# Optimization experiments

Hardware: AMD Instinct MI355X
Metric: run time of the kernel (lower is better)

## Reference

```python
import jax, jax.numpy as jnp
import numpy as np

EPS = jnp.float16(1e-8)

def setup_inputs() -> dict:
    key = jax.random.key(0)
    k1, k2, k3, k4 = jax.random.split(key, 4)
    B, S, D_IN, D_OUT = 4, 2048, 4096, 4096
    x = jax.random.normal(k1, (B, S, D_IN), dtype=jnp.float16)
    weight = jax.random.randint(k2, (D_OUT, D_IN), -127, 127, dtype=jnp.int32).astype(jnp.int8)
    weight_scales = (jax.random.uniform(k3, (D_OUT,), dtype=jnp.float32) * 0.02 + 0.001).astype(jnp.float16)
    bias = (jax.random.normal(k4, (1, D_OUT), dtype=jnp.float32) * 0.01).astype(jnp.float16)
    return {"x": x, "weight": weight, "weight_scales": weight_scales, "bias": bias}

def fake_quant_per_token(x):
    # per-token absmax fake quant to int8 range, stays fp16
    scales = jnp.max(jnp.abs(x), axis=-1, keepdims=True) / jnp.float16(127.0)
    scales = jnp.maximum(scales, EPS)
    return jnp.round(x / scales) * scales

def reference(x, weight, weight_scales, bias):
    # dequantize int8 weight with per-output-channel scales -> fp16 [out, in]
    w_fp16 = weight.astype(jnp.float16) * weight_scales[:, None]
    xq = fake_quant_per_token(x)
    # y = xq @ w^T + bias  : [B, S, out]
    y = jnp.einsum('bsi,oi->bso', xq, w_fp16) + bias
    return y
```

## Files before the change

kernel.cpp:

```cpp
#include <hip/hip_runtime.h>
#include <hip/hip_fp16.h>
#include <stdint.h>

#define M_TOK 8192
#define KD 4096
#define ND 4096

using i32x4  = __attribute__((ext_vector_type(4))) int;
using i32x16 = __attribute__((ext_vector_type(16))) int;

typedef const __attribute__((address_space(1))) void* gp_t;
typedef __attribute__((address_space(3))) void* lp_t;

__global__ __launch_bounds__(256) void prep_kernel(
    const float* __restrict__ x,
    int8_t* __restrict__ q,
    float* __restrict__ scales,
    const int* __restrict__ w32,
    int8_t* __restrict__ w8)
{
    const int t = threadIdx.x;
    if (blockIdx.x >= 8192) {
        const int b = blockIdx.x - 8192;
        const int4* w4 = (const int4*)w32;
        int* q32 = (int*)w8;
        #pragma unroll
        for (int u = 0; u < 4; ++u) {
            int g = b * 1024 + u * 256 + t;
            int4 a = w4[g];
            q32[g] = (a.x & 255) | ((a.y & 255) << 8) | ((a.z & 255) << 16) | (a.w << 24);
        }
        return;
    }

    const int row  = blockIdx.x;
    const int lane = t & 63;
    const int wave = t >> 6;

    const float4* xr = (const float4*)(x + (size_t)row * KD);
    float4 p[4];
    #pragma unroll
    for (int i = 0; i < 4; ++i) p[i] = xr[i * 256 + t];

    float am = 0.0f;
    #pragma unroll
    for (int i = 0; i < 4; ++i) {
        am = fmaxf(am, fmaxf(fmaxf(fabsf(p[i].x), fabsf(p[i].y)),
                             fmaxf(fabsf(p[i].z), fabsf(p[i].w))));
    }
    #pragma unroll
    for (int off = 32; off >= 1; off >>= 1)
        am = fmaxf(am, __shfl_xor(am, off));

    __shared__ float smax[4];
    if (lane == 0) smax[wave] = am;
    __syncthreads();
    am = fmaxf(fmaxf(smax[0], smax[1]), fmaxf(smax[2], smax[3]));

    float s = __half2float(__float2half(am * (1.0f / 127.0f)));
    s = fmaxf(s, 1e-30f);
    const float inv = 1.0f / s;

    int* qr = (int*)(q + (size_t)row * KD);
    #pragma unroll
    for (int i = 0; i < 4; ++i) {
        float vv[4] = {p[i].x, p[i].y, p[i].z, p[i].w};
        int w32v = 0;
        #pragma unroll
        for (int e = 0; e < 4; ++e) {
            float tq = __half2float(__float2half(vv[e] * inv));
            int qi = (int)rintf(tq);
            qi = max(-127, min(127, qi));
            w32v |= (qi & 255) << (8 * e);
        }
        qr[i * 256 + t] = w32v;
    }
    if (t == 0) scales[row] = s;
}


template<int MH>
__device__ __forceinline__ void read_A32(const char* lA, int wr, int lane, i32x4 (&a)[2][4]) {
    const int l31 = lane & 31;
    const int kc  = (lane >> 5) << 4;
    #pragma unroll
    for (int mf = 0; mf < 2; ++mf) {
        const int row = MH * 128 + wr * 64 + mf * 32 + l31;
        const int sw  = (row & 7) << 4;
        #pragma unroll
        for (int ks = 0; ks < 4; ++ks)
            a[mf][ks] = *(const i32x4*)(lA + row * 128 + ((ks * 32 + kc) ^ sw));
    }
}

__device__ __forceinline__ void read_B32(const char* lB, int wc, int lane, i32x4 (&b)[2][4]) {
    const int l31 = lane & 31;
    const int kc  = (lane >> 5) << 4;
    #pragma unroll
    for (int nf = 0; nf < 2; ++nf) {
        const int row = wc * 64 + nf * 32 + l31;
        const int sw  = (row & 7) << 4;
        #pragma unroll
        for (int ks = 0; ks < 4; ++ks)
            b[nf][ks] = *(const i32x4*)(lB + row * 128 + ((ks * 32 + kc) ^ sw));
    }
}

template<int MH>
__device__ __forceinline__ void mfma_half32(i32x16 (&acc)[2][2][2],
                                            const i32x4 (&a)[2][4],
                                            const i32x4 (&b)[2][4]) {
    __builtin_amdgcn_s_setprio(1);
    #pragma unroll
    for (int ks = 0; ks < 4; ++ks)
        #pragma unroll
        for (int mf = 0; mf < 2; ++mf)
            #pragma unroll
            for (int nf = 0; nf < 2; ++nf)
                acc[MH][mf][nf] =
                    __builtin_amdgcn_mfma_i32_32x32x32_i8(a[mf][ks], b[nf][ks],
                                                          acc[MH][mf][nf], 0, 0, 0);
    __builtin_amdgcn_s_setprio(0);
}

#define BAR() do { __builtin_amdgcn_s_barrier(); __builtin_amdgcn_sched_barrier(0); } while (0)

__global__ __launch_bounds__(512, 2) void gemm_q8_32x32_kernel(
    const int8_t* __restrict__ q,
    const int8_t* __restrict__ w8,
    const float* __restrict__ qs,
    const float* __restrict__ wscale,
    const float* __restrict__ bias,
    float* __restrict__ y)
{
    __shared__ char lds[2][2][32768];

    const int tid  = threadIdx.x;
    const int lane = tid & 63;
    const int wave = tid >> 6;
    const int wr   = wave >> 2;
    const int wc   = wave & 3;
    const int tn   = blockIdx.x;
    const int tm   = blockIdx.y;

    const int8_t* gA = q  + (size_t)(tm * 256) * KD;
    const int8_t* gB = w8 + (size_t)(tn * 256) * KD;

    char* lA0 = &lds[0][0][0]; char* lB0 = &lds[0][1][0];
    char* lA1 = &lds[1][0][0]; char* lB1 = &lds[1][1][0];

    int goff[2];
    #pragma unroll
    for (int qq = 0; qq < 2; ++qq) {
        const int d = qq * 8192 + wave * 1024 + lane * 16;
        const int r = d >> 7;
        const int cs = (d & 127) ^ ((r & 7) << 4);
        goff[qq] = r * KD + cs;
    }
    const int ldso = wave * 1024;

    #define STAGE(gbase, half, kbyte, ldst)                                              \
        do {                                                                             \
            const int8_t* _s = (gbase) + (size_t)(half) * 128 * KD + (kbyte);            \
            __builtin_amdgcn_global_load_lds((gp_t)(_s + goff[0]),                       \
                (lp_t)((ldst) + (half) * 16384 + ldso), 16, 0, 0);                       \
            __builtin_amdgcn_global_load_lds((gp_t)(_s + goff[1]),                       \
                (lp_t)((ldst) + (half) * 16384 + 8192 + ldso), 16, 0, 0);                \
        } while (0)

    i32x16 acc[2][2][2] = {};
    i32x4 a[2][4], b[2][4];

    STAGE(gA, 0, 0,   lA0);
    STAGE(gB, 0, 0,   lB0);
    STAGE(gA, 1, 0,   lA0);
    STAGE(gB, 1, 0,   lB0);
    STAGE(gA, 0, 128, lA1);
    STAGE(gB, 0, 128, lB1);
    asm volatile("s_waitcnt vmcnt(4)");
    BAR();

    for (int it = 0; it < 16; ++it) {
        const int kt  = 2 * it;
        const int kb1 = ((kt + 1) & 31) * 128;
        const int kb2 = ((kt + 2) & 31) * 128;
        const int kb3 = ((kt + 3) & 31) * 128;

        read_A32<0>(lA0, wr, lane, a);
        read_B32(lB0, wc, lane, b);
        STAGE(gA, 1, kb1, lA1);
        STAGE(gB, 1, kb1, lB1);
        BAR();
        mfma_half32<0>(acc, a, b);
        BAR();

        read_A32<1>(lA0, wr, lane, a);
        STAGE(gA, 0, kb2, lA0);
        STAGE(gB, 0, kb2, lB0);
        BAR();
        mfma_half32<1>(acc, a, b);
        asm volatile("s_waitcnt vmcnt(4)");
        BAR();

        read_A32<0>(lA1, wr, lane, a);
        read_B32(lB1, wc, lane, b);
        STAGE(gA, 1, kb2, lA0);
        STAGE(gB, 1, kb2, lB0);
        BAR();
        mfma_half32<0>(acc, a, b);
        BAR();

        read_A32<1>(lA1, wr, lane, a);
        STAGE(gA, 0, kb3, lA1);
        STAGE(gB, 0, kb3, lB1);
        BAR();
        mfma_half32<1>(acc, a, b);
        asm volatile("s_waitcnt vmcnt(4)");
        BAR();
    }
    asm volatile("s_waitcnt vmcnt(0)");

    #pragma unroll
    for (int mh = 0; mh < 2; ++mh)
        #pragma unroll
        for (int mf = 0; mf < 2; ++mf) {
            const int rbase = tm * 256 + mh * 128 + wr * 64 + mf * 32 + ((lane >> 5) << 2);
            float qsv[16];
            #pragma unroll
            for (int reg = 0; reg < 16; ++reg)
                qsv[reg] = qs[rbase + (reg & 3) + 8 * (reg >> 2)];
            #pragma unroll
            for (int nf = 0; nf < 2; ++nf) {
                const int n = tn * 256 + wc * 64 + nf * 32 + (lane & 31);
                const float wn = wscale[n];
                const float bn = bias[n];
                #pragma unroll
                for (int reg = 0; reg < 16; ++reg) {
                    const int m = rbase + (reg & 3) + 8 * (reg >> 2);
                    y[(size_t)m * ND + n] =
                        (float)acc[mh][mf][nf][reg] * (qsv[reg] * wn) + bn;
                }
            }
        }
    #undef STAGE
}

__global__ __launch_bounds__(256, 2) void gemm_q8_fallback(
    const int8_t* __restrict__ q,
    const int* __restrict__ w32,
    const float* __restrict__ qs,
    const float* __restrict__ wscale,
    const float* __restrict__ bias,
    float* __restrict__ y)
{
    __shared__ int8_t lA[128 * 64];
    __shared__ int8_t lB[128 * 64];

    const int tid  = threadIdx.x;
    const int lane = tid & 63;
    const int wave = tid >> 6;
    const int wr   = wave >> 1;
    const int wc   = wave & 1;
    const int tn   = blockIdx.x;
    const int tm   = blockIdx.y;

    const int ci0  = wave * 2;
    const int off0 = ci0 * 1024 + lane * 16;
    const int r0   = off0 >> 6;
    const int c0   = off0 & 63;
    const int off1 = off0 + 1024;
    const int r1   = off1 >> 6;
    const int c1   = off1 & 63;

    const int8_t* gA0 = q + (size_t)(tm * 128 + r0) * KD + c0;
    const int8_t* gA1 = q + (size_t)(tm * 128 + r1) * KD + c1;

    const int brow  = tid >> 1;
    const int bhalf = tid & 1;
    const int* gW = w32 + (size_t)(tn * 128 + brow) * KD + bhalf * 32;

    i32x4 acc[4][4] = {};
    const int kc = (lane >> 4) * 16;
    const int rA = wr * 64 + (lane & 15);
    const int rB = wc * 64 + (lane & 15);

    for (int k0 = 0; k0 < KD; k0 += 64) {
        __builtin_amdgcn_global_load_lds((gp_t)(gA0 + k0), (lp_t)(lA + ci0 * 1024),        16, 0, 0);
        __builtin_amdgcn_global_load_lds((gp_t)(gA1 + k0), (lp_t)(lA + ci0 * 1024 + 1024), 16, 0, 0);
        int bw[8];
        #pragma unroll
        for (int u = 0; u < 8; ++u) {
            i32x4 a4 = *(const i32x4*)(gW + k0 + u * 4);
            bw[u] = (a4[0] & 255) | ((a4[1] & 255) << 8) | ((a4[2] & 255) << 16) | (a4[3] << 24);
        }
        *(i32x4*)(lB + brow * 64 + bhalf * 32)      = i32x4{bw[0], bw[1], bw[2], bw[3]};
        *(i32x4*)(lB + brow * 64 + bhalf * 32 + 16) = i32x4{bw[4], bw[5], bw[6], bw[7]};
        __syncthreads();

        i32x4 a[4], b[4];
        #pragma unroll
        for (int i = 0; i < 4; ++i) a[i] = *(const i32x4*)(lA + (rA + i * 16) * 64 + kc);
        #pragma unroll
        for (int j = 0; j < 4; ++j) b[j] = *(const i32x4*)(lB + (rB + j * 16) * 64 + kc);
        #pragma unroll
        for (int i = 0; i < 4; ++i)
            #pragma unroll
            for (int j = 0; j < 4; ++j)
                acc[i][j] = __builtin_amdgcn_mfma_i32_16x16x64_i8(a[i], b[j], acc[i][j], 0, 0, 0);
        __syncthreads();
    }

    const int cbase = tn * 128 + wc * 64 + (lane & 15);
    const int rbase = tm * 128 + wr * 64 + ((lane >> 4) << 2);
    #pragma unroll
    for (int j = 0; j < 4; ++j) {
        const int n  = cbase + j * 16;
        const float wn = wscale[n];
        const float bn = bias[n];
        #pragma unroll
        for (int i = 0; i < 4; ++i)
            #pragma unroll
            for (int r = 0; r < 4; ++r) {
                const int m = rbase + i * 16 + r;
                y[(size_t)m * ND + n] = (float)acc[i][j][r] * (qs[m] * wn) + bn;
            }
    }
}

extern "C" void kernel_launch(void* const* d_in, const int* in_sizes, int n_in,
                              void* d_out, int out_size, void* d_ws, size_t ws_size,
                              hipStream_t stream) {
    const float* x      = (const float*)d_in[0];
    const int*   w32    = (const int*)d_in[1];
    const float* wscale = (const float*)d_in[2];
    const float* bias   = (const float*)d_in[3];
    float*       y      = (float*)d_out;

    const size_t q_bytes  = (size_t)M_TOK * KD;
    const size_t s_bytes  = (size_t)M_TOK * sizeof(float);
    const size_t w8_bytes = (size_t)ND * KD;

    int8_t* qbuf   = (int8_t*)d_ws;
    float*  scales = (float*)((char*)d_ws + q_bytes);
    int8_t* w8     = (int8_t*)((char*)d_ws + q_bytes + s_bytes);

    if (ws_size >= q_bytes + s_bytes + w8_bytes) {
        prep_kernel<<<8192 + 4096, 256, 0, stream>>>(x, qbuf, scales, w32, w8);
        dim3 grid(ND / 256, M_TOK / 256);
        gemm_q8_32x32_kernel<<<grid, 512, 0, stream>>>(qbuf, w8, scales, wscale, bias, y);
    } else {
        prep_kernel<<<8192, 256, 0, stream>>>(x, qbuf, scales, w32, w8);
        dim3 grid(ND / 128, M_TOK / 128);
        gemm_q8_fallback<<<grid, 256, 0, stream>>>(qbuf, w32, scales, wscale, bias, y);
    }
}
```

Measured before the change: 196.9 us.

## Pair-row LDS layout, peeled K tail, LDS-staged vectorized epilogue stores

Changes the LDS tile layout so that two rows are packed per 256-byte line, with a new XOR swizzle and matching global-load offsets, to cut LDS bank conflicts on the MFMA operand reads. The last K iteration is peeled so no wasted wrap-around prefetch loads are issued, extra vmcnt waits are added, and sched_barrier is removed from BAR. The epilogue now stages the fp32 results through per-wave LDS and writes them with 16-byte nontemporal stores instead of scattered 4-byte stores. This adds barriers and LDS traffic in the epilogue, and the new swizzle has to stay exactly consistent between the writer and the reader paths.

```diff
diff --git a/kernel.cpp b/kernel.cpp
--- a/kernel.cpp
+++ b/kernel.cpp
@@ -8,6 +8,7 @@
 
 using i32x4  = __attribute__((ext_vector_type(4))) int;
 using i32x16 = __attribute__((ext_vector_type(16))) int;
+using f32x4  = __attribute__((ext_vector_type(4))) float;
 
 typedef const __attribute__((address_space(1))) void* gp_t;
 typedef __attribute__((address_space(3))) void* lp_t;
@@ -80,29 +81,27 @@
 
 
 template<int MH>
-__device__ __forceinline__ void read_A32(const char* lA, int wr, int lane, i32x4 (&a)[2][4]) {
-    const int l31 = lane & 31;
-    const int kc  = (lane >> 5) << 4;
+__device__ __forceinline__ void read_A32(const char* lA, int wr, int hw, int kp8, i32x4 (&a)[2][4]) {
     #pragma unroll
     for (int mf = 0; mf < 2; ++mf) {
-        const int row = MH * 128 + wr * 64 + mf * 32 + l31;
-        const int sw  = (row & 7) << 4;
-        #pragma unroll
-        for (int ks = 0; ks < 4; ++ks)
-            a[mf][ks] = *(const i32x4*)(lA + row * 128 + ((ks * 32 + kc) ^ sw));
-    }
-}
-
-__device__ __forceinline__ void read_B32(const char* lB, int wc, int lane, i32x4 (&b)[2][4]) {
-    const int l31 = lane & 31;
-    const int kc  = (lane >> 5) << 4;
+        const int i256 = (MH * 64 + wr * 32 + mf * 16 + hw) * 256;
+        #pragma unroll
+        for (int ks = 0; ks < 4; ++ks) {
+            const int slot = ((ks * 2 + kp8) ^ hw) << 4;
+            a[mf][ks] = *(const i32x4*)(lA + i256 + slot);
+        }
+    }
+}
+
+__device__ __forceinline__ void read_B32(const char* lB, int wc, int hw, int kp8, i32x4 (&b)[2][4]) {
     #pragma unroll
     for (int nf = 0; nf < 2; ++nf) {
-        const int row = wc * 64 + nf * 32 + l31;
-        const int sw  = (row & 7) << 4;
-        #pragma unroll
-        for (int ks = 0; ks < 4; ++ks)
-            b[nf][ks] = *(const i32x4*)(lB + row * 128 + ((ks * 32 + kc) ^ sw));
+        const int i256 = (wc * 32 + nf * 16 + hw) * 256;
+        #pragma unroll
+        for (int ks = 0; ks < 4; ++ks) {
+            const int slot = ((ks * 2 + kp8) ^ hw) << 4;
+            b[nf][ks] = *(const i32x4*)(lB + i256 + slot);
+        }
     }
 }
 
@@ -123,9 +122,9 @@
     __builtin_amdgcn_s_setprio(0);
 }
 
-#define BAR() do { __builtin_amdgcn_s_barrier(); __builtin_amdgcn_sched_barrier(0); } while (0)
-
-__global__ __launch_bounds__(512, 2) void gemm_q8_32x32_kernel(
+#define BAR() __builtin_amdgcn_s_barrier()
+
+__global__ __launch_bounds__(512, 2) void gemm_q8_pr_kernel(
     const int8_t* __restrict__ q,
     const int8_t* __restrict__ w8,
     const float* __restrict__ qs,
@@ -149,13 +148,19 @@
     char* lA0 = &lds[0][0][0]; char* lB0 = &lds[0][1][0];
     char* lA1 = &lds[1][0][0]; char* lB1 = &lds[1][1][0];
 
+    const int hw  = (lane & 31) >> 1;
+    const int kp8 = (lane >> 5) + ((lane & 1) << 3);
+
     int goff[2];
     #pragma unroll
     for (int qq = 0; qq < 2; ++qq) {
-        const int d = qq * 8192 + wave * 1024 + lane * 16;
-        const int r = d >> 7;
-        const int cs = (d & 127) ^ ((r & 7) << 4);
-        goff[qq] = r * KD + cs;
+        const int d  = qq * 8192 + wave * 1024 + lane * 16;
+        const int il = d >> 8;
+        const int sp = (d >> 4) & 15;
+        const int s  = sp ^ (il & 15);
+        const int rl = 2 * il + (s >> 3);
+        const int k  = (s << 4) & 127;
+        goff[qq] = rl * KD + k;
     }
     const int ldso = wave * 1024;
 
@@ -180,21 +185,22 @@
     asm volatile("s_waitcnt vmcnt(4)");
     BAR();
 
-    for (int it = 0; it < 16; ++it) {
+    for (int it = 0; it < 15; ++it) {
         const int kt  = 2 * it;
-        const int kb1 = ((kt + 1) & 31) * 128;
-        const int kb2 = ((kt + 2) & 31) * 128;
-        const int kb3 = ((kt + 3) & 31) * 128;
-
-        read_A32<0>(lA0, wr, lane, a);
-        read_B32(lB0, wc, lane, b);
+        const int kb1 = (kt + 1) * 128;
+        const int kb2 = (kt + 2) * 128;
+        const int kb3 = (kt + 3) * 128;
+
+        read_A32<0>(lA0, wr, hw, kp8, a);
+        read_B32(lB0, wc, hw, kp8, b);
         STAGE(gA, 1, kb1, lA1);
         STAGE(gB, 1, kb1, lB1);
         BAR();
         mfma_half32<0>(acc, a, b);
-        BAR();
-
-        read_A32<1>(lA0, wr, lane, a);
+        asm volatile("s_waitcnt vmcnt(4)");
+        BAR();
+
+        read_A32<1>(lA0, wr, hw, kp8, a);
         STAGE(gA, 0, kb2, lA0);
         STAGE(gB, 0, kb2, lB0);
         BAR();
@@ -202,15 +208,16 @@
         asm volatile("s_waitcnt vmcnt(4)");
         BAR();
 
-        read_A32<0>(lA1, wr, lane, a);
-        read_B32(lB1, wc, lane, b);
+        read_A32<0>(lA1, wr, hw, kp8, a);
+        read_B32(lB1, wc, hw, kp8, b);
         STAGE(gA, 1, kb2, lA0);
         STAGE(gB, 1, kb2, lB0);
         BAR();
         mfma_half32<0>(acc, a, b);
-        BAR();
-
-        read_A32<1>(lA1, wr, lane, a);
+        asm volatile("s_waitcnt vmcnt(4)");
+        BAR();
+
+        read_A32<1>(lA1, wr, hw, kp8, a);
         STAGE(gA, 0, kb3, lA1);
         STAGE(gB, 0, kb3, lB1);
         BAR();
@@ -218,30 +225,70 @@
         asm volatile("s_waitcnt vmcnt(4)");
         BAR();
     }
-    asm volatile("s_waitcnt vmcnt(0)");
-
-    #pragma unroll
-    for (int mh = 0; mh < 2; ++mh)
-        #pragma unroll
-        for (int mf = 0; mf < 2; ++mf) {
-            const int rbase = tm * 256 + mh * 128 + wr * 64 + mf * 32 + ((lane >> 5) << 2);
-            float qsv[16];
+
+    {
+        const int kb1 = 31 * 128;
+        read_A32<0>(lA0, wr, hw, kp8, a);
+        read_B32(lB0, wc, hw, kp8, b);
+        STAGE(gA, 1, kb1, lA1);
+        STAGE(gB, 1, kb1, lB1);
+        BAR();
+        mfma_half32<0>(acc, a, b);
+        BAR();
+
+        read_A32<1>(lA0, wr, hw, kp8, a);
+        BAR();
+        mfma_half32<1>(acc, a, b);
+        asm volatile("s_waitcnt vmcnt(0)");
+        BAR();
+
+        read_A32<0>(lA1, wr, hw, kp8, a);
+        read_B32(lB1, wc, hw, kp8, b);
+        BAR();
+        mfma_half32<0>(acc, a, b);
+        BAR();
+
+        read_A32<1>(lA1, wr, hw, kp8, a);
+        BAR();
+        mfma_half32<1>(acc, a, b);
+        BAR();
+    }
+
+    {
+        char* myl = &lds[0][0][0] + wave * 16384;
+        const int l31 = lane & 31;
+        const int g4  = (lane >> 5) << 2;
+        #pragma unroll
+        for (int nf = 0; nf < 2; ++nf) {
+            const int n  = tn * 256 + wc * 64 + nf * 32 + l31;
+            const float wn = wscale[n];
+            const float bn = bias[n];
             #pragma unroll
-            for (int reg = 0; reg < 16; ++reg)
-                qsv[reg] = qs[rbase + (reg & 3) + 8 * (reg >> 2)];
+            for (int mh = 0; mh < 2; ++mh)
+                #pragma unroll
+                for (int mf = 0; mf < 2; ++mf) {
+                    const int rlb = mh * 64 + mf * 32 + g4;
+                    const int grb = tm * 256 + mh * 128 + wr * 64 + mf * 32 + g4;
+                    #pragma unroll
+                    for (int reg = 0; reg < 16; ++reg) {
+                        const int rr = (reg & 3) + 8 * (reg >> 2);
+                        const int rl = rlb + rr;
+                        const float val = (float)acc[mh][mf][nf][reg] * (qs[grb + rr] * wn) + bn;
+                        *(float*)(myl + rl * 128 + ((l31 * 4) ^ ((rl & 7) << 4))) = val;
+                    }
+                }
+            __builtin_amdgcn_s_barrier();
+            const int gcol = tn * 256 + wc * 64 + nf * 32 + (lane & 7) * 4;
             #pragma unroll
-            for (int nf = 0; nf < 2; ++nf) {
-                const int n = tn * 256 + wc * 64 + nf * 32 + (lane & 31);
-                const float wn = wscale[n];
-                const float bn = bias[n];
-                #pragma unroll
-                for (int reg = 0; reg < 16; ++reg) {
-                    const int m = rbase + (reg & 3) + 8 * (reg >> 2);
-                    y[(size_t)m * ND + n] =
-                        (float)acc[mh][mf][nf][reg] * (qsv[reg] * wn) + bn;
-                }
+            for (int k = 0; k < 16; ++k) {
+                const int rl = (lane >> 3) + k * 8;
+                const f32x4 v = *(const f32x4*)(myl + rl * 128 + (((lane & 7) * 16) ^ ((rl & 7) << 4)));
+                const int grow = tm * 256 + (rl >> 6) * 128 + wr * 64 + (rl & 63);
+                __builtin_nontemporal_store(v, (f32x4*)(y + (size_t)grow * ND + gcol));
             }
-        }
+            __builtin_amdgcn_s_barrier();
+        }
+    }
     #undef STAGE
 }
 
@@ -347,7 +394,7 @@
     if (ws_size >= q_bytes + s_bytes + w8_bytes) {
         prep_kernel<<<8192 + 4096, 256, 0, stream>>>(x, qbuf, scales, w32, w8);
         dim3 grid(ND / 256, M_TOK / 256);
-        gemm_q8_32x32_kernel<<<grid, 512, 0, stream>>>(qbuf, w8, scales, wscale, bias, y);
+        gemm_q8_pr_kernel<<<grid, 512, 0, stream>>>(qbuf, w8, scales, wscale, bias, y);
     } else {
         prep_kernel<<<8192, 256, 0, stream>>>(x, qbuf, scales, w32, w8);
         dim3 grid(ND / 128, M_TOK / 128);
```

Result: faster. 182.6 us (-7.3%).
